# Kernel optimization log

Hardware: AMD Instinct MI355X
Metric: run time of the kernel (lower is better)

Reference implementation:

```python
import jax, jax.numpy as jnp
import numpy as np

V = 30      # vocab
D = 512     # hidden


def gru_cell(x, h, W_ih, W_hh, b_ih, b_hh):
    # PyTorch GRU cell math. x: [B, in], h: [B, D]
    gi = x @ W_ih.T + b_ih          # [B, 3D]
    gh = h @ W_hh.T + b_hh          # [B, 3D]
    i_r, i_z, i_n = jnp.split(gi, 3, axis=-1)
    h_r, h_z, h_n = jnp.split(gh, 3, axis=-1)
    r = jax.nn.sigmoid(i_r + h_r)
    z = jax.nn.sigmoid(i_z + h_z)
    n = jnp.tanh(i_n + r * h_n)
    return (1.0 - z) * n + z * h


def setup_inputs() -> dict:
    key = jax.random.key(0)
    ks = jax.random.split(key, 16)
    B, T, S = 64, 200, 1024
    p = 0.05  # param scale
    return {
        "initial_decoder_hidden": jax.random.normal(ks[0], (2, B, D), jnp.float32),
        "targets": jax.random.randint(ks[1], (B, T), 0, V),
        "encoder_outputs": jax.random.normal(ks[2], (B, S, D), jnp.float32),
        "W_ih0": jax.random.normal(ks[3], (3 * D, V), jnp.float32) * p,
        "W_hh0": jax.random.normal(ks[4], (3 * D, D), jnp.float32) * p,
        "b_ih0": jax.random.normal(ks[5], (3 * D,), jnp.float32) * p,
        "b_hh0": jax.random.normal(ks[6], (3 * D,), jnp.float32) * p,
        "W_ih1": jax.random.normal(ks[7], (3 * D, D), jnp.float32) * p,
        "W_hh1": jax.random.normal(ks[8], (3 * D, D), jnp.float32) * p,
        "b_ih1": jax.random.normal(ks[9], (3 * D,), jnp.float32) * p,
        "b_hh1": jax.random.normal(ks[10], (3 * D,), jnp.float32) * p,
        "W_out": jax.random.normal(ks[11], (D, 2 * D), jnp.float32) * p,
        "W_tok": jax.random.normal(ks[12], (V, D), jnp.float32) * p,
        "b_tok": jax.random.normal(ks[13], (V,), jnp.float32) * p,
    }


def reference(initial_decoder_hidden, targets, encoder_outputs,
              W_ih0, W_hh0, b_ih0, b_hh0,
              W_ih1, W_hh1, b_ih1, b_hh1,
              W_out, W_tok, b_tok):
    # Teacher-forced decode. Original feeds one_hot(targets[:,0]) at t=0,
    # then one_hot(targets[:,t]) AFTER step t, i.e. step t>0 consumes
    # one_hot(targets[:, t-1]).
    B, T = targets.shape
    idx = jnp.concatenate([targets[:, :1], targets[:, :-1]], axis=1)  # [B, T]
    xs = jax.nn.one_hot(idx, V, dtype=jnp.float32)                    # [B, T, V]
    xs = jnp.swapaxes(xs, 0, 1)                                       # [T, B, V]

    mem = encoder_outputs  # [B, S, D]

    def step(carry, x):
        h0, h1 = carry
        h0 = gru_cell(x, h0, W_ih0, W_hh0, b_ih0, b_hh0)
        h1 = gru_cell(h0, h1, W_ih1, W_hh1, b_ih1, b_hh1)
        q = h1                                              # [B, D] top-layer hidden
        scores = jnp.einsum("bd,bsd->bs", q, mem)           # dot attention
        a = jax.nn.softmax(scores, axis=-1)                 # [B, S]
        c = jnp.einsum("bs,bsd->bd", a, mem)                # context [B, D]
        attn_h = jnp.tanh(jnp.concatenate([c, q], axis=-1) @ W_out.T)  # [B, D]
        logits = attn_h @ W_tok.T + b_tok                   # [B, V]
        return (h0, h1), logits

    h_init = (initial_decoder_hidden[0], initial_decoder_hidden[1])
    _, logits = jax.lax.scan(step, h_init, xs)              # [T, B, V]
    return jnp.swapaxes(logits, 0, 1)                       # [B, T, V]
```

## Files before the change

kernel.cpp:

```cpp
#include <hip/hip_runtime.h>

#define TT 200
#define SS 1024
#define DD 512
#define VV 30
#define BB 64
#define BBDD (BB*DD)

#define WS_H0   0
#define WS_GI   (2*BBDD)
#define WS_H1A  (WS_GI + 2*1536*64)
#define WS_CALL (WS_H1A + 200*BBDD)

typedef __attribute__((ext_vector_type(4))) float f4;

__device__ __forceinline__ float dot4(f4 a, f4 b) {
  return a.x*b.x + a.y*b.y + a.z*b.z + a.w*b.w;
}
__device__ __forceinline__ float sigmoidf_(float x) { return 1.f/(1.f + __expf(-x)); }

__device__ __forceinline__ void gl_lds16(const void* g, void* l) {
  __builtin_amdgcn_global_load_lds(
      (const __attribute__((address_space(1))) unsigned int*)g,
      (__attribute__((address_space(3))) unsigned int*)l,
      16, 0, 0);
}

__device__ __forceinline__ void stage64(const float* src, float* TILE, int wv, int lane) {
  #pragma unroll
  for (int rr = 0; rr < 8; ++rr) {
    const int row = wv*8 + rr;
    const float* g = src + (size_t)row*DD + lane*4;
    gl_lds16(g,       TILE + row*516);
    gl_lds16(g + 256, TILE + row*516 + 256);
  }
}

__device__ __forceinline__ void wave_dots(const float* TILE, const float* W, const float* bias,
                                          float* GH, int w_id, int wv, int lane) {
  const int c0 = wv*3, c1 = c0+1, c2 = c0+2;
  const int R0 = __builtin_amdgcn_readfirstlane(((c0>>3)<<9) + w_id*8 + (c0&7));
  const int R1 = __builtin_amdgcn_readfirstlane(((c1>>3)<<9) + w_id*8 + (c1&7));
  const int R2 = __builtin_amdgcn_readfirstlane(((c2>>3)<<9) + w_id*8 + (c2&7));
  const f4* w0 = (const f4*)(W + (size_t)R0*DD);
  const f4* w1 = (const f4*)(W + (size_t)R1*DD);
  const f4* w2 = (const f4*)(W + (size_t)R2*DD);
  const f4* hv4 = (const f4*)TILE + (size_t)lane*129;
  float a0=0.f, a1=0.f, a2=0.f;
  #pragma unroll 4
  for (int kq = 0; kq < 128; ++kq) {
    f4 h = hv4[kq];
    a0 += dot4(h, w0[kq]); a1 += dot4(h, w1[kq]); a2 += dot4(h, w2[kq]);
  }
  GH[c0*64 + lane] = a0 + bias[R0];
  GH[c1*64 + lane] = a1 + bias[R1];
  GH[c2*64 + lane] = a2 + bias[R2];
}

__device__ __forceinline__ void wave_dots_g(const float* TILE, const float* W, const float* bias,
                                            float* gi, int w_id, int wv, int lane) {
  const int c0 = wv*3, c1 = c0+1, c2 = c0+2;
  const int R0 = __builtin_amdgcn_readfirstlane(((c0>>3)<<9) + w_id*8 + (c0&7));
  const int R1 = __builtin_amdgcn_readfirstlane(((c1>>3)<<9) + w_id*8 + (c1&7));
  const int R2 = __builtin_amdgcn_readfirstlane(((c2>>3)<<9) + w_id*8 + (c2&7));
  const f4* w0 = (const f4*)(W + (size_t)R0*DD);
  const f4* w1 = (const f4*)(W + (size_t)R1*DD);
  const f4* w2 = (const f4*)(W + (size_t)R2*DD);
  const f4* hv4 = (const f4*)TILE + (size_t)lane*129;
  float a0=0.f, a1=0.f, a2=0.f;
  #pragma unroll 4
  for (int kq = 0; kq < 128; ++kq) {
    f4 h = hv4[kq];
    a0 += dot4(h, w0[kq]); a1 += dot4(h, w1[kq]); a2 += dot4(h, w2[kq]);
  }
  gi[(size_t)R0*64 + lane] = a0 + bias[R0];
  gi[(size_t)R1*64 + lane] = a1 + bias[R1];
  gi[(size_t)R2*64 + lane] = a2 + bias[R2];
}

__launch_bounds__(512, 1)
__global__ void k_gru0(const float* __restrict__ h0prev, const int* __restrict__ targets,
                       const float* __restrict__ W_ih0, const float* __restrict__ W_hh0,
                       const float* __restrict__ b_ih0, const float* __restrict__ b_hh0,
                       float* __restrict__ h0out, int tokcol) {
  __shared__ float SM[34560];
  float* const TILE = SM;
  float* const GHX  = SM + 33024;
  const int tid = threadIdx.x, bid = blockIdx.x;
  const int lane = tid & 63, wv = tid >> 6;
  stage64(h0prev, TILE, wv, lane);
  __syncthreads();
  wave_dots(TILE, W_hh0, b_hh0, GHX, bid, wv, lane);
  __syncthreads();
  const int dl = tid >> 6, bb = tid & 63, d = bid*8 + dl;
  const int tok = targets[bb*TT + tokcol];
  float gir = W_ih0[(size_t)d*VV + tok]          + b_ih0[d];
  float giz = W_ih0[(size_t)(DD + d)*VV + tok]   + b_ih0[DD + d];
  float gin = W_ih0[(size_t)(2*DD + d)*VV + tok] + b_ih0[2*DD + d];
  float r_ = sigmoidf_(gir + GHX[(0*8 + dl)*64 + bb]);
  float z_ = sigmoidf_(giz + GHX[(1*8 + dl)*64 + bb]);
  float n_ = tanhf(gin + r_*GHX[(2*8 + dl)*64 + bb]);
  float h0old = TILE[bb*516 + d];
  h0out[(size_t)bb*DD + d] = (1.f - z_)*n_ + z_*h0old;
}

__launch_bounds__(512, 1)
__global__ void k_pro1(const float* __restrict__ h0buf0, const int* __restrict__ targets,
                       const float* __restrict__ W_ih0, const float* __restrict__ W_hh0,
                       const float* __restrict__ b_ih0, const float* __restrict__ b_hh0,
                       const float* __restrict__ W_ih1, const float* __restrict__ b_ih1,
                       float* __restrict__ h0buf1, float* __restrict__ gibuf0) {
  __shared__ float SM[34560];
  float* const TILE = SM;
  float* const GHX  = SM + 33024;
  const int tid = threadIdx.x, bid = blockIdx.x;
  const int lane = tid & 63, wv = tid >> 6;
  stage64(h0buf0, TILE, wv, lane);
  __syncthreads();
  if (bid < 64) {
    wave_dots(TILE, W_hh0, b_hh0, GHX, bid, wv, lane);
    __syncthreads();
    const int dl = tid >> 6, bb = tid & 63, d = bid*8 + dl;
    const int tok = targets[bb*TT + 0];
    float gir = W_ih0[(size_t)d*VV + tok]          + b_ih0[d];
    float giz = W_ih0[(size_t)(DD + d)*VV + tok]   + b_ih0[DD + d];
    float gin = W_ih0[(size_t)(2*DD + d)*VV + tok] + b_ih0[2*DD + d];
    float r_ = sigmoidf_(gir + GHX[(0*8 + dl)*64 + bb]);
    float z_ = sigmoidf_(giz + GHX[(1*8 + dl)*64 + bb]);
    float n_ = tanhf(gin + r_*GHX[(2*8 + dl)*64 + bb]);
    float h0old = TILE[bb*516 + d];
    h0buf1[(size_t)bb*DD + d] = (1.f - z_)*n_ + z_*h0old;
  } else {
    wave_dots_g(TILE, W_ih1, b_ih1, gibuf0, bid - 64, wv, lane);
  }
}

__launch_bounds__(512, 1)
__global__ void k_chain(const float* __restrict__ h0rd,
                        float*       __restrict__ h0wr,
                        const float* __restrict__ h1src,
                        float*       __restrict__ h1dst,
                        const float* __restrict__ gird,
                        float*       __restrict__ giwr,
                        const int*   __restrict__ targets,
                        const float* __restrict__ W_ih0, const float* __restrict__ W_hh0,
                        const float* __restrict__ b_ih0, const float* __restrict__ b_hh0,
                        const float* __restrict__ W_hh1, const float* __restrict__ b_hh1,
                        const float* __restrict__ W_ih1, const float* __restrict__ b_ih1,
                        int t) {
  __shared__ float SM[34560];
  float* const TILE = SM;
  float* const GHX  = SM + 33024;
  const int tid = threadIdx.x, bid = blockIdx.x;
  const int lane = tid & 63, wv = tid >> 6;
  const int dl = tid >> 6, bb = tid & 63;

  if (bid < 64) {
    if (t <= 197) {
      const int d = bid*8 + dl;
      stage64(h0rd, TILE, wv, lane);
      __syncthreads();
      wave_dots(TILE, W_hh0, b_hh0, GHX, bid, wv, lane);
      __syncthreads();
      const int tok = targets[bb*TT + (t + 1)];
      float gir = W_ih0[(size_t)d*VV + tok]          + b_ih0[d];
      float giz = W_ih0[(size_t)(DD + d)*VV + tok]   + b_ih0[DD + d];
      float gin = W_ih0[(size_t)(2*DD + d)*VV + tok] + b_ih0[2*DD + d];
      float r_ = sigmoidf_(gir + GHX[(0*8 + dl)*64 + bb]);
      float z_ = sigmoidf_(giz + GHX[(1*8 + dl)*64 + bb]);
      float n_ = tanhf(gin + r_*GHX[(2*8 + dl)*64 + bb]);
      float h0old = TILE[bb*516 + d];
      h0wr[(size_t)bb*DD + d] = (1.f - z_)*n_ + z_*h0old;
    }
  } else if (bid < 128) {
    const int w_id = bid - 64;
    const int d = w_id*8 + dl;
    stage64(h1src, TILE, wv, lane);
    __syncthreads();
    wave_dots(TILE, W_hh1, b_hh1, GHX, w_id, wv, lane);
    float h1old = TILE[bb*516 + d];
    __syncthreads();
    float gir = gird[(size_t)(0*DD + d)*64 + bb];
    float giz = gird[(size_t)(1*DD + d)*64 + bb];
    float gin = gird[(size_t)(2*DD + d)*64 + bb];
    float r_ = sigmoidf_(gir + GHX[(0*8 + dl)*64 + bb]);
    float z_ = sigmoidf_(giz + GHX[(1*8 + dl)*64 + bb]);
    float n_ = tanhf(gin + r_*GHX[(2*8 + dl)*64 + bb]);
    h1dst[(size_t)bb*DD + d] = (1.f - z_)*n_ + z_*h1old;
  } else {
    if (t <= 198) {
      stage64(h0rd, TILE, wv, lane);
      __syncthreads();
      wave_dots_g(TILE, W_ih1, b_ih1, giwr, bid - 128, wv, lane);
    }
  }
}

__launch_bounds__(512, 1)
__global__ void k_attn_all(const float* __restrict__ h1a, const float* __restrict__ mem,
                           float* __restrict__ call) {
  __shared__ float SM[2*16*520 + 8*80];
  float* const SCR = SM + 2*16*520;
  const int tid = threadIdx.x, bid = blockIdx.x;
  const int lane = tid & 63, wv = tid >> 6;
  const int b  = bid / 5;
  const int tt = bid % 5;
  const int r0 = wv*5;

  f4 qa[5], qb[5];
  #pragma unroll
  for (int r = 0; r < 5; ++r) {
    const size_t base = ((size_t)(tt*40 + r0 + r)*BB + b)*DD + lane*8;
    qa[r] = *(const f4*)(h1a + base);
    qb[r] = *(const f4*)(h1a + base + 4);
  }
  f4 aa[5], ab[5];
  float m[5], l[5];
  #pragma unroll
  for (int r = 0; r < 5; ++r) { aa[r] = (f4)0.f; ab[r] = (f4)0.f; m[r] = -3e38f; l[r] = 0.f; }

  const float* msrc = mem + (size_t)b*SS*DD;
  #pragma unroll
  for (int rr = 0; rr < 2; ++rr) {
    const int row = wv*2 + rr;
    const float* g = msrc + (size_t)row*DD + lane*4;
    gl_lds16(g,       SM + row*520);
    gl_lds16(g + 256, SM + row*520 + 256);
  }
  __syncthreads();

  int buf = 0;
  for (int tl = 0; tl < 64; ++tl) {
    if (tl + 1 < 64) {
      float* nb = SM + (buf^1)*16*520;
      #pragma unroll
      for (int rr = 0; rr < 2; ++rr) {
        const int row = wv*2 + rr;
        const float* g = msrc + (size_t)(tl+1)*16*DD + (size_t)row*DD + lane*4;
        gl_lds16(g,       nb + row*520);
        gl_lds16(g + 256, nb + row*520 + 256);
      }
    }
    const float* mt = SM + buf*16*520;

    for (int s = 0; s < 16; ++s) {
      const f4 ma = *(const f4*)&mt[s*520 + lane*8];
      const f4 mb = *(const f4*)&mt[s*520 + lane*8 + 4];
      float p[5];
      #pragma unroll
      for (int r = 0; r < 5; ++r) p[r] = dot4(ma, qa[r]) + dot4(mb, qb[r]);
      #pragma unroll
      for (int off = 32; off; off >>= 1) {
        #pragma unroll
        for (int r = 0; r < 5; ++r) p[r] += __shfl_xor(p[r], off);
      }
      if (lane == 0) {
        #pragma unroll
        for (int r = 0; r < 5; ++r) SCR[wv*80 + r*16 + s] = p[r];
      }
    }
    float mnew[5], esc[5];
    #pragma unroll
    for (int r = 0; r < 5; ++r) {
      float mx = -3e38f;
      #pragma unroll
      for (int s = 0; s < 16; ++s) mx = fmaxf(mx, SCR[wv*80 + r*16 + s]);
      mnew[r] = fmaxf(m[r], mx);
      esc[r]  = __expf(m[r] - mnew[r]);
      aa[r] *= esc[r]; ab[r] *= esc[r]; l[r] *= esc[r];
      m[r] = mnew[r];
    }
    for (int s = 0; s < 16; ++s) {
      const f4 ma = *(const f4*)&mt[s*520 + lane*8];
      const f4 mb = *(const f4*)&mt[s*520 + lane*8 + 4];
      #pragma unroll
      for (int r = 0; r < 5; ++r) {
        const float w = __expf(SCR[wv*80 + r*16 + s] - m[r]);
        aa[r] += w*ma; ab[r] += w*mb; l[r] += w;
      }
    }
    __syncthreads();
    buf ^= 1;
  }

  #pragma unroll
  for (int r = 0; r < 5; ++r) {
    const float inv = 1.f / l[r];
    const size_t base = ((size_t)(tt*40 + r0 + r)*BB + b)*DD + lane*8;
    *(f4*)(call + base)     = aa[r]*inv;
    *(f4*)(call + base + 4) = ab[r]*inv;
  }
}

__launch_bounds__(512, 1)
__global__ void k_outproj(const float* __restrict__ call, const float* __restrict__ h1a,
                          const float* __restrict__ W_out, const float* __restrict__ W_tok,
                          const float* __restrict__ b_tok, float* __restrict__ out) {
  __shared__ float SM[4352 + 33024];
  float* const XR = SM;
  float* const AH = SM + 4352;
  const int tid = threadIdx.x, bid = blockIdx.x;
  const int lane = tid & 63, wv = tid >> 6;
  const int rowbase = bid * 64;

  float acc[8][8];
  #pragma unroll
  for (int r = 0; r < 8; ++r)
    #pragma unroll
    for (int j = 0; j < 8; ++j) acc[r][j] = 0.f;

  for (int kc = 0; kc < 16; ++kc) {
    __syncthreads();
    {
      const int row = tid >> 3;
      const int kp  = (tid & 7) * 8;
      const int k   = kc*64 + kp;
      const size_t grow = (size_t)(rowbase + row) * DD;
      const float* src = (k < DD) ? (call + grow + k) : (h1a + grow + (k - DD));
      f4 v0 = *(const f4*)src;
      f4 v1 = *(const f4*)(src + 4);
      *(f4*)&XR[row*68 + kp]     = v0;
      *(f4*)&XR[row*68 + kp + 4] = v1;
    }
    __syncthreads();
    for (int k4 = 0; k4 < 16; ++k4) {
      f4 w4[8];
      #pragma unroll
      for (int j = 0; j < 8; ++j)
        w4[j] = *(const f4*)&W_out[(size_t)(lane*8 + j)*(2*DD) + kc*64 + k4*4];
      #pragma unroll
      for (int r = 0; r < 8; ++r) {
        const f4 x4 = *(const f4*)&XR[(wv*8 + r)*68 + k4*4];
        #pragma unroll
        for (int j = 0; j < 8; ++j) acc[r][j] += dot4(x4, w4[j]);
      }
    }
  }
  #pragma unroll
  for (int r = 0; r < 8; ++r) {
    f4 t0, t1;
    t0.x = tanhf(acc[r][0]); t0.y = tanhf(acc[r][1]); t0.z = tanhf(acc[r][2]); t0.w = tanhf(acc[r][3]);
    t1.x = tanhf(acc[r][4]); t1.y = tanhf(acc[r][5]); t1.z = tanhf(acc[r][6]); t1.w = tanhf(acc[r][7]);
    *(f4*)&AH[(wv*8 + r)*516 + lane*8]     = t0;
    *(f4*)&AH[(wv*8 + r)*516 + lane*8 + 4] = t1;
  }
  __syncthreads();
  const int v = tid & 31;
  const int rq = tid >> 5;
  if (v < VV) {
    for (int it = 0; it < 4; ++it) {
      const int row = rq + it*16;
      float s = 0.f;
      const f4* ar = (const f4*)&AH[row*516];
      const f4* wt = (const f4*)&W_tok[(size_t)v*DD];
      #pragma unroll 4
      for (int k4 = 0; k4 < 128; ++k4) s += dot4(ar[k4], wt[k4]);
      const int gr = rowbase + row;
      const int t = gr >> 6, b = gr & 63;
      out[((size_t)b*TT + t)*VV + v] = s + b_tok[v];
    }
  }
}

extern "C" void kernel_launch(void* const* d_in, const int* in_sizes, int n_in,
                              void* d_out, int out_size, void* d_ws, size_t ws_size,
                              hipStream_t stream) {
  const float* h_init = (const float*)d_in[0];
  const int*   targets= (const int*)d_in[1];
  const float* mem    = (const float*)d_in[2];
  const float* W_ih0  = (const float*)d_in[3];
  const float* W_hh0  = (const float*)d_in[4];
  const float* b_ih0  = (const float*)d_in[5];
  const float* b_hh0  = (const float*)d_in[6];
  const float* W_ih1  = (const float*)d_in[7];
  const float* W_hh1  = (const float*)d_in[8];
  const float* b_ih1  = (const float*)d_in[9];
  const float* b_hh1  = (const float*)d_in[10];
  const float* W_out  = (const float*)d_in[11];
  const float* W_tok  = (const float*)d_in[12];
  const float* b_tok  = (const float*)d_in[13];
  float* out = (float*)d_out;
  float* ws  = (float*)d_ws;

  float* h0b  = ws + WS_H0;
  float* gib  = ws + WS_GI;
  float* h1a  = ws + WS_H1A;
  float* call = ws + WS_CALL;

  hipLaunchKernelGGL(k_gru0, dim3(64), dim3(512), 0, stream,
                     h_init, targets, W_ih0, W_hh0, b_ih0, b_hh0, h0b, 0);
  hipLaunchKernelGGL(k_pro1, dim3(128), dim3(512), 0, stream,
                     h0b, targets, W_ih0, W_hh0, b_ih0, b_hh0,
                     W_ih1, b_ih1, h0b + BBDD, gib);

  for (int t = 0; t < TT; ++t) {
    const float* h0rd = h0b + (size_t)((t + 1) & 1)*BBDD;
    float*       h0wr = h0b + (size_t)(t & 1)*BBDD;
    const float* h1src= (t == 0) ? (h_init + BBDD) : (h1a + (size_t)(t - 1)*BBDD);
    float*       h1dst= h1a + (size_t)t*BBDD;
    const float* gird = gib + (size_t)(t & 1)*(1536*64);
    float*       giwr = gib + (size_t)((t + 1) & 1)*(1536*64);
    hipLaunchKernelGGL(k_chain, dim3(192), dim3(512), 0, stream,
                       h0rd, h0wr, h1src, h1dst, gird, giwr, targets,
                       W_ih0, W_hh0, b_ih0, b_hh0, W_hh1, b_hh1, W_ih1, b_ih1, t);
  }

  hipLaunchKernelGGL(k_attn_all, dim3(320), dim3(512), 0, stream, h1a, mem, call);

  hipLaunchKernelGGL(k_outproj, dim3(200), dim3(512), 0, stream,
                     call, h1a, W_out, W_tok, b_tok, out);
}
```

Before: 5.579 ms.

## Replace per-step chain launches with persistent cooperative kernel and grid barrier

The 200 per-timestep k_chain launches are replaced by a single cooperative persistent kernel of 192 blocks. The blocks synchronise between steps with a custom flag-based grid barrier, and cross-block data moves through coherent (sc0 sc1) global loads and stores, which removes per-launch overhead from the serial recurrence. If the cooperative launch fails, the code falls back to the original loop. Separately, the attention kernel's per-lane access pattern changes from contiguous 8-float chunks to two strided 4-float halves. The barrier adds spin-wait latency, and the coherent staging bypasses the async LDS loads.

```diff
diff --git a/kernel.cpp b/kernel.cpp
--- a/kernel.cpp
+++ b/kernel.cpp
@@ -6,11 +6,15 @@
 #define VV 30
 #define BB 64
 #define BBDD (BB*DD)
-
-#define WS_H0   0
-#define WS_GI   (2*BBDD)
-#define WS_H1A  (WS_GI + 2*1536*64)
-#define WS_CALL (WS_H1A + 200*BBDD)
+#define CNBLK 192
+
+#define WS_GSLOT 0
+#define WS_GBF   (192*32)
+#define WS_SLOTS_UINTS (2*192*32)
+#define WS_H0    12288
+#define WS_GI    (WS_H0 + 2*BBDD)
+#define WS_H1A   (WS_GI + 2*1536*64)
+#define WS_CALL  (WS_H1A + 200*BBDD)
 
 typedef __attribute__((ext_vector_type(4))) float f4;
 
@@ -34,6 +38,51 @@
     gl_lds16(g,       TILE + row*516);
     gl_lds16(g + 256, TILE + row*516 + 256);
   }
+}
+
+__device__ __forceinline__ void coh_store1(float* p, float v) {
+  asm volatile("global_store_dword %0, %1, off sc0 sc1" :: "v"(p), "v"(v) : "memory");
+}
+__device__ __forceinline__ void coh_load3(const float* p0, const float* p1, const float* p2,
+                                          float& r0, float& r1, float& r2) {
+  asm volatile(
+    "global_load_dword %0, %3, off sc0 sc1\n\t"
+    "global_load_dword %1, %4, off sc0 sc1\n\t"
+    "global_load_dword %2, %5, off sc0 sc1\n\t"
+    "s_waitcnt vmcnt(0)"
+    : "=&v"(r0), "=&v"(r1), "=&v"(r2)
+    : "v"(p0), "v"(p1), "v"(p2) : "memory");
+}
+__device__ __forceinline__ void coh_load8x4(const float* g, int stridef, f4 (&r)[8]) {
+  const float *a1 = g +   (size_t)stridef, *a2 = g + 2*(size_t)stridef,
+              *a3 = g + 3*(size_t)stridef, *a4 = g + 4*(size_t)stridef,
+              *a5 = g + 5*(size_t)stridef, *a6 = g + 6*(size_t)stridef,
+              *a7 = g + 7*(size_t)stridef;
+  asm volatile(
+    "global_load_dwordx4 %0, %8, off sc0 sc1\n\t"
+    "global_load_dwordx4 %1, %9, off sc0 sc1\n\t"
+    "global_load_dwordx4 %2, %10, off sc0 sc1\n\t"
+    "global_load_dwordx4 %3, %11, off sc0 sc1\n\t"
+    "global_load_dwordx4 %4, %12, off sc0 sc1\n\t"
+    "global_load_dwordx4 %5, %13, off sc0 sc1\n\t"
+    "global_load_dwordx4 %6, %14, off sc0 sc1\n\t"
+    "global_load_dwordx4 %7, %15, off sc0 sc1\n\t"
+    "s_waitcnt vmcnt(0)"
+    : "=&v"(r[0]), "=&v"(r[1]), "=&v"(r[2]), "=&v"(r[3]),
+      "=&v"(r[4]), "=&v"(r[5]), "=&v"(r[6]), "=&v"(r[7])
+    : "v"(g), "v"(a1), "v"(a2), "v"(a3), "v"(a4), "v"(a5), "v"(a6), "v"(a7)
+    : "memory");
+}
+__device__ __forceinline__ void stage64_coh(const float* src, float* TILE, int tid) {
+  f4 r[8];
+  const int c4 = (tid & 127) * 4;
+  const int rb = tid >> 7;
+  coh_load8x4(src + (size_t)tid*4, 2048, r);
+  #pragma unroll
+  for (int k = 0; k < 8; ++k) *(f4*)&TILE[(rb + 4*k)*516 + c4] = r[k];
+  coh_load8x4(src + (size_t)tid*4 + 8*2048, 2048, r);
+  #pragma unroll
+  for (int k = 0; k < 8; ++k) *(f4*)&TILE[(rb + 4*(k+8))*516 + c4] = r[k];
 }
 
 __device__ __forceinline__ void wave_dots(const float* TILE, const float* W, const float* bias,
@@ -78,6 +127,52 @@
   gi[(size_t)R2*64 + lane] = a2 + bias[R2];
 }
 
+__device__ __forceinline__ void wave_dots_g_coh(const float* TILE, const float* W, const float* bias,
+                                                float* gi, int w_id, int wv, int lane) {
+  const int c0 = wv*3, c1 = c0+1, c2 = c0+2;
+  const int R0 = __builtin_amdgcn_readfirstlane(((c0>>3)<<9) + w_id*8 + (c0&7));
+  const int R1 = __builtin_amdgcn_readfirstlane(((c1>>3)<<9) + w_id*8 + (c1&7));
+  const int R2 = __builtin_amdgcn_readfirstlane(((c2>>3)<<9) + w_id*8 + (c2&7));
+  const f4* w0 = (const f4*)(W + (size_t)R0*DD);
+  const f4* w1 = (const f4*)(W + (size_t)R1*DD);
+  const f4* w2 = (const f4*)(W + (size_t)R2*DD);
+  const f4* hv4 = (const f4*)TILE + (size_t)lane*129;
+  float a0=0.f, a1=0.f, a2=0.f;
+  #pragma unroll 4
+  for (int kq = 0; kq < 128; ++kq) {
+    f4 h = hv4[kq];
+    a0 += dot4(h, w0[kq]); a1 += dot4(h, w1[kq]); a2 += dot4(h, w2[kq]);
+  }
+  coh_store1(&gi[(size_t)R0*64 + lane], a0 + bias[R0]);
+  coh_store1(&gi[(size_t)R1*64 + lane], a1 + bias[R1]);
+  coh_store1(&gi[(size_t)R2*64 + lane], a2 + bias[R2]);
+}
+
+__device__ __forceinline__ void gridbar(unsigned* gslot, unsigned* gbf,
+                                        int bid, int tid, unsigned target) {
+  __syncthreads();
+  if (tid == 0)
+    __hip_atomic_store(&gslot[bid*32], target, __ATOMIC_RELAXED, __HIP_MEMORY_SCOPE_AGENT);
+  if (bid == 0) {
+    if (tid < 64) {
+      for (;;) {
+        unsigned v0 = __hip_atomic_load(&gslot[(tid      )*32], __ATOMIC_RELAXED, __HIP_MEMORY_SCOPE_AGENT);
+        unsigned v1 = __hip_atomic_load(&gslot[(tid +  64)*32], __ATOMIC_RELAXED, __HIP_MEMORY_SCOPE_AGENT);
+        unsigned v2 = __hip_atomic_load(&gslot[(tid + 128)*32], __ATOMIC_RELAXED, __HIP_MEMORY_SCOPE_AGENT);
+        if (__all(v0 >= target && v1 >= target && v2 >= target)) break;
+        __builtin_amdgcn_s_sleep(2);
+      }
+    }
+    __syncthreads();
+    if (tid >= 1 && tid < CNBLK)
+      __hip_atomic_store(&gbf[tid*32], target, __ATOMIC_RELAXED, __HIP_MEMORY_SCOPE_AGENT);
+  } else if (tid == 0) {
+    while (__hip_atomic_load(&gbf[bid*32], __ATOMIC_RELAXED, __HIP_MEMORY_SCOPE_AGENT) < target)
+      __builtin_amdgcn_s_sleep(2);
+  }
+  __syncthreads();
+}
+
 __launch_bounds__(512, 1)
 __global__ void k_gru0(const float* __restrict__ h0prev, const int* __restrict__ targets,
                        const float* __restrict__ W_ih0, const float* __restrict__ W_hh0,
@@ -136,13 +231,10 @@
 }
 
 __launch_bounds__(512, 1)
-__global__ void k_chain(const float* __restrict__ h0rd,
-                        float*       __restrict__ h0wr,
-                        const float* __restrict__ h1src,
-                        float*       __restrict__ h1dst,
-                        const float* __restrict__ gird,
-                        float*       __restrict__ giwr,
-                        const int*   __restrict__ targets,
+__global__ void k_chain(const float* __restrict__ h0rd, float* __restrict__ h0wr,
+                        const float* __restrict__ h1src, float* __restrict__ h1dst,
+                        const float* __restrict__ gird, float* __restrict__ giwr,
+                        const int* __restrict__ targets,
                         const float* __restrict__ W_ih0, const float* __restrict__ W_hh0,
                         const float* __restrict__ b_ih0, const float* __restrict__ b_hh0,
                         const float* __restrict__ W_hh1, const float* __restrict__ b_hh1,
@@ -197,6 +289,73 @@
 }
 
 __launch_bounds__(512, 1)
+__global__ void k_chain_pers(const float* h_init, const int* targets,
+                             const float* W_ih0, const float* W_hh0,
+                             const float* b_ih0, const float* b_hh0,
+                             const float* W_hh1, const float* b_hh1,
+                             const float* W_ih1, const float* b_ih1,
+                             float* h0b, float* gib, float* h1a,
+                             unsigned* gslot, unsigned* gbf) {
+  __shared__ float SM[34560];
+  float* const TILE = SM;
+  float* const GHX  = SM + 33024;
+  const int tid = threadIdx.x, bid = blockIdx.x;
+  const int lane = tid & 63, wv = tid >> 6;
+  const int dl = tid >> 6, bb = tid & 63;
+
+  for (int t = 0; t < TT; ++t) {
+    const float* h0rd = h0b + (size_t)((t + 1) & 1)*BBDD;
+    float*       h0wr = h0b + (size_t)(t & 1)*BBDD;
+    const float* h1src= (t == 0) ? (h_init + BBDD) : (h1a + (size_t)(t - 1)*BBDD);
+    float*       h1dst= h1a + (size_t)t*BBDD;
+    const float* gird = gib + (size_t)(t & 1)*(1536*64);
+    float*       giwr = gib + (size_t)((t + 1) & 1)*(1536*64);
+
+    if (bid < 64) {
+      if (t <= 197) {
+        const int d = bid*8 + dl;
+        stage64_coh(h0rd, TILE, tid);
+        __syncthreads();
+        wave_dots(TILE, W_hh0, b_hh0, GHX, bid, wv, lane);
+        __syncthreads();
+        const int tok = targets[bb*TT + (t + 1)];
+        float gir = W_ih0[(size_t)d*VV + tok]          + b_ih0[d];
+        float giz = W_ih0[(size_t)(DD + d)*VV + tok]   + b_ih0[DD + d];
+        float gin = W_ih0[(size_t)(2*DD + d)*VV + tok] + b_ih0[2*DD + d];
+        float r_ = sigmoidf_(gir + GHX[(0*8 + dl)*64 + bb]);
+        float z_ = sigmoidf_(giz + GHX[(1*8 + dl)*64 + bb]);
+        float n_ = tanhf(gin + r_*GHX[(2*8 + dl)*64 + bb]);
+        float h0old = TILE[bb*516 + d];
+        coh_store1(&h0wr[(size_t)bb*DD + d], (1.f - z_)*n_ + z_*h0old);
+      }
+    } else if (bid < 128) {
+      const int w_id = bid - 64;
+      const int d = w_id*8 + dl;
+      stage64_coh(h1src, TILE, tid);
+      __syncthreads();
+      wave_dots(TILE, W_hh1, b_hh1, GHX, w_id, wv, lane);
+      float h1old = TILE[bb*516 + d];
+      __syncthreads();
+      float gir, giz, gin;
+      coh_load3(&gird[(size_t)(0*DD + d)*64 + bb],
+                &gird[(size_t)(1*DD + d)*64 + bb],
+                &gird[(size_t)(2*DD + d)*64 + bb], gir, giz, gin);
+      float r_ = sigmoidf_(gir + GHX[(0*8 + dl)*64 + bb]);
+      float z_ = sigmoidf_(giz + GHX[(1*8 + dl)*64 + bb]);
+      float n_ = tanhf(gin + r_*GHX[(2*8 + dl)*64 + bb]);
+      coh_store1(&h1dst[(size_t)bb*DD + d], (1.f - z_)*n_ + z_*h1old);
+    } else {
+      if (t <= 198) {
+        stage64_coh(h0rd, TILE, tid);
+        __syncthreads();
+        wave_dots_g_coh(TILE, W_ih1, b_ih1, giwr, bid - 128, wv, lane);
+      }
+    }
+    gridbar(gslot, gbf, bid, tid, (unsigned)(t + 1));
+  }
+}
+
+__launch_bounds__(512, 1)
 __global__ void k_attn_all(const float* __restrict__ h1a, const float* __restrict__ mem,
                            float* __restrict__ call) {
   __shared__ float SM[2*16*520 + 8*80];
@@ -208,11 +367,12 @@
   const int r0 = wv*5;
 
   f4 qa[5], qb[5];
+  size_t rbase[5];
   #pragma unroll
   for (int r = 0; r < 5; ++r) {
-    const size_t base = ((size_t)(tt*40 + r0 + r)*BB + b)*DD + lane*8;
-    qa[r] = *(const f4*)(h1a + base);
-    qb[r] = *(const f4*)(h1a + base + 4);
+    rbase[r] = ((size_t)(tt*40 + r0 + r)*BB + b)*DD;
+    qa[r] = *(const f4*)(h1a + rbase[r] + lane*4);
+    qb[r] = *(const f4*)(h1a + rbase[r] + lane*4 + 256);
   }
   f4 aa[5], ab[5];
   float m[5], l[5];
@@ -244,8 +404,8 @@
     const float* mt = SM + buf*16*520;
 
     for (int s = 0; s < 16; ++s) {
-      const f4 ma = *(const f4*)&mt[s*520 + lane*8];
-      const f4 mb = *(const f4*)&mt[s*520 + lane*8 + 4];
+      const f4 ma = *(const f4*)&mt[s*520 + lane*4];
+      const f4 mb = *(const f4*)&mt[s*520 + lane*4 + 256];
       float p[5];
       #pragma unroll
       for (int r = 0; r < 5; ++r) p[r] = dot4(ma, qa[r]) + dot4(mb, qb[r]);
@@ -271,8 +431,8 @@
       m[r] = mnew[r];
     }
     for (int s = 0; s < 16; ++s) {
-      const f4 ma = *(const f4*)&mt[s*520 + lane*8];
-      const f4 mb = *(const f4*)&mt[s*520 + lane*8 + 4];
+      const f4 ma = *(const f4*)&mt[s*520 + lane*4];
+      const f4 mb = *(const f4*)&mt[s*520 + lane*4 + 256];
       #pragma unroll
       for (int r = 0; r < 5; ++r) {
         const float w = __expf(SCR[wv*80 + r*16 + s] - m[r]);
@@ -286,9 +446,8 @@
   #pragma unroll
   for (int r = 0; r < 5; ++r) {
     const float inv = 1.f / l[r];
-    const size_t base = ((size_t)(tt*40 + r0 + r)*BB + b)*DD + lane*8;
-    *(f4*)(call + base)     = aa[r]*inv;
-    *(f4*)(call + base + 4) = ab[r]*inv;
+    *(f4*)(call + rbase[r] + lane*4)       = aa[r]*inv;
+    *(f4*)(call + rbase[r] + lane*4 + 256) = ab[r]*inv;
   }
 }
 
@@ -382,10 +541,14 @@
   float* out = (float*)d_out;
   float* ws  = (float*)d_ws;
 
+  unsigned* gslot = (unsigned*)ws + WS_GSLOT;
+  unsigned* gbf   = (unsigned*)ws + WS_GBF;
   float* h0b  = ws + WS_H0;
   float* gib  = ws + WS_GI;
   float* h1a  = ws + WS_H1A;
   float* call = ws + WS_CALL;
+
+  hipMemsetAsync(d_ws, 0, WS_SLOTS_UINTS * sizeof(unsigned), stream);
 
   hipLaunchKernelGGL(k_gru0, dim3(64), dim3(512), 0, stream,
                      h_init, targets, W_ih0, W_hh0, b_ih0, b_hh0, h0b, 0);
@@ -393,16 +556,27 @@
                      h0b, targets, W_ih0, W_hh0, b_ih0, b_hh0,
                      W_ih1, b_ih1, h0b + BBDD, gib);
 
-  for (int t = 0; t < TT; ++t) {
-    const float* h0rd = h0b + (size_t)((t + 1) & 1)*BBDD;
-    float*       h0wr = h0b + (size_t)(t & 1)*BBDD;
-    const float* h1src= (t == 0) ? (h_init + BBDD) : (h1a + (size_t)(t - 1)*BBDD);
-    float*       h1dst= h1a + (size_t)t*BBDD;
-    const float* gird = gib + (size_t)(t & 1)*(1536*64);
-    float*       giwr = gib + (size_t)((t + 1) & 1)*(1536*64);
-    hipLaunchKernelGGL(k_chain, dim3(192), dim3(512), 0, stream,
-                       h0rd, h0wr, h1src, h1dst, gird, giwr, targets,
-                       W_ih0, W_hh0, b_ih0, b_hh0, W_hh1, b_hh1, W_ih1, b_ih1, t);
+  {
+    void* args[] = { (void*)&h_init, (void*)&targets,
+                     (void*)&W_ih0, (void*)&W_hh0, (void*)&b_ih0, (void*)&b_hh0,
+                     (void*)&W_hh1, (void*)&b_hh1, (void*)&W_ih1, (void*)&b_ih1,
+                     (void*)&h0b, (void*)&gib, (void*)&h1a,
+                     (void*)&gslot, (void*)&gbf };
+    hipError_t err = hipLaunchCooperativeKernel((const void*)k_chain_pers,
+                                                dim3(CNBLK), dim3(512), args, 0, stream);
+    if (err != hipSuccess) {
+      for (int t = 0; t < TT; ++t) {
+        const float* h0rd = h0b + (size_t)((t + 1) & 1)*BBDD;
+        float*       h0wr = h0b + (size_t)(t & 1)*BBDD;
+        const float* h1src= (t == 0) ? (h_init + BBDD) : (h1a + (size_t)(t - 1)*BBDD);
+        float*       h1dst= h1a + (size_t)t*BBDD;
+        const float* gird = gib + (size_t)(t & 1)*(1536*64);
+        float*       giwr = gib + (size_t)((t + 1) & 1)*(1536*64);
+        hipLaunchKernelGGL(k_chain, dim3(192), dim3(512), 0, stream,
+                           h0rd, h0wr, h1src, h1dst, gird, giwr, targets,
+                           W_ih0, W_hh0, b_ih0, b_hh0, W_hh1, b_hh1, W_ih1, b_ih1, t);
+      }
+    }
   }
 
   hipLaunchKernelGGL(k_attn_all, dim3(320), dim3(512), 0, stream, h1a, mem, call);
```

New measurement: 8.009 ms. +43.6%, slower.

## Restructure attention score computation to avoid full-wave shuffle reductions

Applied to the files above, without the earlier changes.

The attention kernel now stages the 40 query rows into LDS and computes scores with 16 groups of 4 lanes, one memory row per group. Each lane reads a rotated (bank-skewed) slice of the row, so the six-level cross-wave shuffle reduction per score is replaced by a two-level reduction within each group. The row padding changes from 520 to 516 floats and the context accumulation now uses contiguous float4 lane indexing. This costs more LDS for the queries and more LDS reads of the query vectors per score.

```diff
diff --git a/kernel.cpp b/kernel.cpp
--- a/kernel.cpp
+++ b/kernel.cpp
@@ -136,13 +136,10 @@
 }
 
 __launch_bounds__(512, 1)
-__global__ void k_chain(const float* __restrict__ h0rd,
-                        float*       __restrict__ h0wr,
-                        const float* __restrict__ h1src,
-                        float*       __restrict__ h1dst,
-                        const float* __restrict__ gird,
-                        float*       __restrict__ giwr,
-                        const int*   __restrict__ targets,
+__global__ void k_chain(const float* __restrict__ h0rd, float* __restrict__ h0wr,
+                        const float* __restrict__ h1src, float* __restrict__ h1dst,
+                        const float* __restrict__ gird, float* __restrict__ giwr,
+                        const int* __restrict__ targets,
                         const float* __restrict__ W_ih0, const float* __restrict__ W_hh0,
                         const float* __restrict__ b_ih0, const float* __restrict__ b_hh0,
                         const float* __restrict__ W_hh1, const float* __restrict__ b_hh1,
@@ -199,80 +196,82 @@
 __launch_bounds__(512, 1)
 __global__ void k_attn_all(const float* __restrict__ h1a, const float* __restrict__ mem,
                            float* __restrict__ call) {
-  __shared__ float SM[2*16*520 + 8*80];
-  float* const SCR = SM + 2*16*520;
+  __shared__ float SM[37792];
+  float* const QL  = SM + 16512;
+  float* const SCR = SM + 37152;
   const int tid = threadIdx.x, bid = blockIdx.x;
   const int lane = tid & 63, wv = tid >> 6;
-  const int b  = bid / 5;
-  const int tt = bid % 5;
-  const int r0 = wv*5;
-
-  f4 qa[5], qb[5];
-  #pragma unroll
-  for (int r = 0; r < 5; ++r) {
-    const size_t base = ((size_t)(tt*40 + r0 + r)*BB + b)*DD + lane*8;
-    qa[r] = *(const f4*)(h1a + base);
-    qb[r] = *(const f4*)(h1a + base + 4);
-  }
-  f4 aa[5], ab[5];
-  float m[5], l[5];
-  #pragma unroll
-  for (int r = 0; r < 5; ++r) { aa[r] = (f4)0.f; ab[r] = (f4)0.f; m[r] = -3e38f; l[r] = 0.f; }
-
+  const int b = bid / 5, tt = bid % 5;
+  const int g = lane >> 2, sub = lane & 3;
+
+  #pragma unroll
+  for (int rr = 0; rr < 5; ++rr) {
+    const int row = wv*5 + rr;
+    const float* src = h1a + ((size_t)(tt*40 + row)*BB + b)*DD + lane*4;
+    gl_lds16(src,       QL + row*516);
+    gl_lds16(src + 256, QL + row*516 + 256);
+  }
   const float* msrc = mem + (size_t)b*SS*DD;
   #pragma unroll
   for (int rr = 0; rr < 2; ++rr) {
     const int row = wv*2 + rr;
-    const float* g = msrc + (size_t)row*DD + lane*4;
-    gl_lds16(g,       SM + row*520);
-    gl_lds16(g + 256, SM + row*520 + 256);
+    const float* gsp = msrc + (size_t)row*DD + lane*4;
+    gl_lds16(gsp,       SM + row*516);
+    gl_lds16(gsp + 256, SM + row*516 + 256);
   }
   __syncthreads();
+
+  f4 aa[5], ab[5]; float m[5], l[5];
+  #pragma unroll
+  for (int r = 0; r < 5; ++r) { aa[r] = (f4)0.f; ab[r] = (f4)0.f; m[r] = -3e38f; l[r] = 0.f; }
 
   int buf = 0;
   for (int tl = 0; tl < 64; ++tl) {
     if (tl + 1 < 64) {
-      float* nb = SM + (buf^1)*16*520;
+      float* nb = SM + (buf^1)*8256;
       #pragma unroll
       for (int rr = 0; rr < 2; ++rr) {
         const int row = wv*2 + rr;
-        const float* g = msrc + (size_t)(tl+1)*16*DD + (size_t)row*DD + lane*4;
-        gl_lds16(g,       nb + row*520);
-        gl_lds16(g + 256, nb + row*520 + 256);
+        const float* gsp = msrc + (size_t)(tl+1)*16*DD + (size_t)row*DD + lane*4;
+        gl_lds16(gsp,       nb + row*516);
+        gl_lds16(gsp + 256, nb + row*516 + 256);
       }
     }
-    const float* mt = SM + buf*16*520;
-
-    for (int s = 0; s < 16; ++s) {
-      const f4 ma = *(const f4*)&mt[s*520 + lane*8];
-      const f4 mb = *(const f4*)&mt[s*520 + lane*8 + 4];
-      float p[5];
-      #pragma unroll
-      for (int r = 0; r < 5; ++r) p[r] = dot4(ma, qa[r]) + dot4(mb, qb[r]);
-      #pragma unroll
-      for (int off = 32; off; off >>= 1) {
-        #pragma unroll
-        for (int r = 0; r < 5; ++r) p[r] += __shfl_xor(p[r], off);
-      }
-      if (lane == 0) {
-        #pragma unroll
-        for (int r = 0; r < 5; ++r) SCR[wv*80 + r*16 + s] = p[r];
-      }
-    }
-    float mnew[5], esc[5];
+    const f4* mtf4 = (const f4*)(SM + buf*8256);
+    const f4* qlf4 = (const f4*)QL;
+
+    float p[5] = {0.f, 0.f, 0.f, 0.f, 0.f};
+    #pragma unroll 4
+    for (int k = 0; k < 32; ++k) {
+      const int idx = sub*32 + ((k + sub) & 31);
+      const f4 mv = mtf4[g*129 + idx];
+      #pragma unroll
+      for (int r = 0; r < 5; ++r)
+        p[r] += dot4(mv, qlf4[(wv*5 + r)*129 + idx]);
+    }
     #pragma unroll
     for (int r = 0; r < 5; ++r) {
-      float mx = -3e38f;
-      #pragma unroll
-      for (int s = 0; s < 16; ++s) mx = fmaxf(mx, SCR[wv*80 + r*16 + s]);
-      mnew[r] = fmaxf(m[r], mx);
-      esc[r]  = __expf(m[r] - mnew[r]);
-      aa[r] *= esc[r]; ab[r] *= esc[r]; l[r] *= esc[r];
-      m[r] = mnew[r];
+      p[r] += __shfl_xor(p[r], 1);
+      p[r] += __shfl_xor(p[r], 2);
+    }
+    if (sub == 0) {
+      #pragma unroll
+      for (int r = 0; r < 5; ++r) SCR[wv*80 + r*16 + g] = p[r];
+    }
+
+    #pragma unroll
+    for (int r = 0; r < 5; ++r) {
+      float mx = SCR[wv*80 + r*16];
+      #pragma unroll
+      for (int s = 1; s < 16; ++s) mx = fmaxf(mx, SCR[wv*80 + r*16 + s]);
+      const float mnew = fmaxf(m[r], mx);
+      const float esc = __expf(m[r] - mnew);
+      aa[r] *= esc; ab[r] *= esc; l[r] *= esc;
+      m[r] = mnew;
     }
     for (int s = 0; s < 16; ++s) {
-      const f4 ma = *(const f4*)&mt[s*520 + lane*8];
-      const f4 mb = *(const f4*)&mt[s*520 + lane*8 + 4];
+      const f4 ma = mtf4[s*129 + lane];
+      const f4 mb = mtf4[s*129 + lane + 64];
       #pragma unroll
       for (int r = 0; r < 5; ++r) {
         const float w = __expf(SCR[wv*80 + r*16 + s] - m[r]);
@@ -286,9 +285,9 @@
   #pragma unroll
   for (int r = 0; r < 5; ++r) {
     const float inv = 1.f / l[r];
-    const size_t base = ((size_t)(tt*40 + r0 + r)*BB + b)*DD + lane*8;
-    *(f4*)(call + base)     = aa[r]*inv;
-    *(f4*)(call + base + 4) = ab[r]*inv;
+    float* dst = call + ((size_t)(tt*40 + wv*5 + r)*BB + b)*DD;
+    *(f4*)(dst + lane*4)       = aa[r]*inv;
+    *(f4*)(dst + lane*4 + 256) = ab[r]*inv;
   }
 }
 
```

Result: faster. 4.650 ms (-16.7%).
